# Kernel optimization log

Measured on AMD Instinct MI355X. Metric: run time of the kernel, lower is better.

Reference implementation:

```python
import jax, jax.numpy as jnp
import numpy as np

D_MODEL = 1024
N_HEADS = 16
D_K = D_MODEL // N_HEADS
B, L = 8, 512


def setup_inputs() -> dict:
    key = jax.random.key(0)
    ks = jax.random.split(key, 12)
    s = 0.02
    return {
        "q": jax.random.normal(ks[0], (B, L, D_MODEL), jnp.float32),
        "k": jax.random.normal(ks[1], (B, L, D_MODEL), jnp.float32),
        "v": jax.random.normal(ks[2], (B, L, D_MODEL), jnp.float32),
        "rel_pos_emb": jax.random.normal(ks[3], (L, L, D_MODEL), jnp.float32) * s,
        "mask": jnp.ones((1, 1, L, L), jnp.int32),
        "Wq": jax.random.normal(ks[4], (D_MODEL, D_MODEL), jnp.float32) * s,
        "bq": jnp.zeros((D_MODEL,), jnp.float32),
        "Wk": jax.random.normal(ks[5], (D_MODEL, D_MODEL), jnp.float32) * s,
        "bk": jnp.zeros((D_MODEL,), jnp.float32),
        "Wv": jax.random.normal(ks[6], (D_MODEL, D_MODEL), jnp.float32) * s,
        "bv": jnp.zeros((D_MODEL,), jnp.float32),
        "Wo": jax.random.normal(ks[7], (D_MODEL, D_MODEL), jnp.float32) * s,
        "bo": jnp.zeros((D_MODEL,), jnp.float32),
    }


def reference(q, k, v, rel_pos_emb, mask, Wq, bq, Wk, bk, Wv, bv, Wo, bo):
    Bn, Ln, D = q.shape
    H, dk = N_HEADS, D // N_HEADS
    # QKV projections (nn.Linear: x @ W^T + b), split heads -> [B,H,L,dk]
    qh = (q @ Wq.T + bq).reshape(Bn, Ln, H, dk).transpose(0, 2, 1, 3)
    kh = (k @ Wk.T + bk).reshape(Bn, Ln, H, dk).transpose(0, 2, 1, 3)
    vh = (v @ Wv.T + bv).reshape(Bn, Ln, H, dk).transpose(0, 2, 1, 3)
    # relative position embeddings -> [H,L,L,dk]
    rel = rel_pos_emb.reshape(Ln, Ln, H, dk).transpose(2, 0, 1, 3)
    scale = 1.0 / jnp.sqrt(jnp.float32(dk))
    scores = jnp.einsum('bhld,bhrd->bhlr', qh, kh) * scale
    scores = scores + jnp.einsum('bhld,hlrd->bhlr', qh, rel)
    scores = jnp.where(mask == 0, jnp.float32(-1e9), scores)
    attn = jax.nn.softmax(scores, axis=-1)  # dropout omitted (eval mode)
    out = jnp.einsum('bhlr,bhrd->bhld', attn, vh)
    out = out.transpose(0, 2, 1, 3).reshape(Bn, Ln, D)
    return out @ Wo.T + bo
```

## Files before the change

### kernel.cpp

```cpp
#include <hip/hip_runtime.h>

typedef __attribute__((ext_vector_type(8))) short short8;
typedef __attribute__((ext_vector_type(4))) float f32x4;
typedef __attribute__((ext_vector_type(4))) unsigned short u16x4;
typedef unsigned int u32;
typedef unsigned short ushort_t;

union frag_u { u32 w[4]; short8 s; };

static __device__ __forceinline__ unsigned short f2bf(float x) {
  union { float f; unsigned u; } v; v.f = x;
  unsigned r = v.u + 0x7fffu + ((v.u >> 16) & 1u);
  return (unsigned short)(r >> 16);
}
static __device__ __forceinline__ float bf2f(unsigned short h) {
  union { unsigned u; float f; } v; v.u = ((unsigned)h) << 16;
  return v.f;
}
static __device__ __forceinline__ u32 pk_bf16(float a, float b) {
  u32 r;
  asm("v_cvt_pk_bf16_f32 %0, %1, %2" : "=v"(r) : "v"(a), "v"(b));
  return r;
}

static __device__ __forceinline__ void gl_lds16(const void* g, void* s) {
  __builtin_amdgcn_global_load_lds(
      (const __attribute__((address_space(1))) void*)g,
      (__attribute__((address_space(3))) void*)s, 16, 0, 0);
}

__global__ __launch_bounds__(256) void to_bf16(const float* __restrict__ src,
                                               ushort_t* __restrict__ dst, int n4) {
  int i = blockIdx.x * blockDim.x + threadIdx.x;
  int stride = gridDim.x * blockDim.x;
  for (; i < n4; i += stride) {
    float4 x = *(const float4*)&src[i * 4];
    u16x4 o;
    o.x = f2bf(x.x); o.y = f2bf(x.y); o.z = f2bf(x.z); o.w = f2bf(x.w);
    *(u16x4*)&dst[i * 4] = o;
  }
}

__global__ __launch_bounds__(256) void split3_bf16(const float* __restrict__ src,
                                                   ushort_t* __restrict__ dst, int n) {
  int i = blockIdx.x * blockDim.x + threadIdx.x;
  int stride = gridDim.x * blockDim.x;
  for (; i < n; i += stride) {
    int r = i >> 10, c = i & 1023;
    float x = src[i];
    unsigned short hi = f2bf(x);
    unsigned short lo = f2bf(x - bf2f(hi));
    ushort_t* row = dst + (size_t)r * 3072;
    row[c] = hi; row[1024 + c] = hi; row[2048 + c] = lo;
  }
}

__global__ __launch_bounds__(256) void gemm_qkv(
    const ushort_t* __restrict__ qbf, const ushort_t* __restrict__ kbf,
    const ushort_t* __restrict__ vbf, const ushort_t* __restrict__ Wqb,
    const ushort_t* __restrict__ Wkb, const ushort_t* __restrict__ Wvb,
    const float* __restrict__ bq, const float* __restrict__ bk,
    const float* __restrict__ bv, float* __restrict__ qh,
    ushort_t* __restrict__ khb, ushort_t* __restrict__ vT) {
  __shared__ ushort_t As[2][128 * 32];
  __shared__ ushort_t Bs[2][128 * 32];
  const int t = threadIdx.x;
  const int lane = t & 63;
  const int w = t >> 6;
  const int wr = w >> 1, wc = w & 1;
  const int bid = blockIdx.x;
  const int mt = bid / 24, ntg = bid % 24;
  const int which = ntg >> 3, nt = ntg & 7;
  const ushort_t* A  = which == 0 ? qbf : which == 1 ? kbf : vbf;
  const ushort_t* Bw = which == 0 ? Wqb : which == 1 ? Wkb : Wvb;
  const float* bias  = which == 0 ? bq  : which == 1 ? bk  : bv;
  const int m0 = mt * 128, n0 = nt * 128;
  const int r16 = lane & 15, kb = lane >> 4;

  f32x4 acc[4][4];
#pragma unroll
  for (int mi = 0; mi < 4; ++mi)
#pragma unroll
    for (int ni = 0; ni < 4; ++ni) acc[mi][ni] = (f32x4){0.f, 0.f, 0.f, 0.f};

  auto STAGE = [&](int buf, int k0) {
#pragma unroll
    for (int i = 0; i < 2; ++i) {
      int c = i * 256 + t;
      int row = c >> 2, kc = (c & 3) * 8;
      gl_lds16(&A[(size_t)(m0 + row) * 1024 + k0 + kc], &As[buf][c * 8]);
      gl_lds16(&Bw[(size_t)(n0 + row) * 1024 + k0 + kc], &Bs[buf][c * 8]);
    }
  };

  STAGE(0, 0);
  __syncthreads();
  int cur = 0;
  for (int kt = 0; kt < 32; ++kt) {
    if (kt + 1 < 32) STAGE(cur ^ 1, (kt + 1) * 32);
    short8 af[4], bf[4];
#pragma unroll
    for (int mi = 0; mi < 4; ++mi)
      af[mi] = *(const short8*)&As[cur][(wr * 64 + mi * 16 + r16) * 32 + kb * 8];
#pragma unroll
    for (int ni = 0; ni < 4; ++ni)
      bf[ni] = *(const short8*)&Bs[cur][(wc * 64 + ni * 16 + r16) * 32 + kb * 8];
#pragma unroll
    for (int mi = 0; mi < 4; ++mi)
#pragma unroll
      for (int ni = 0; ni < 4; ++ni)
        acc[mi][ni] = __builtin_amdgcn_mfma_f32_16x16x32_bf16(af[mi], bf[ni], acc[mi][ni], 0, 0, 0);
    __syncthreads();
    cur ^= 1;
  }

  const int rowD = (lane >> 4) * 4;
#pragma unroll
  for (int mi = 0; mi < 4; ++mi) {
#pragma unroll
    for (int ni = 0; ni < 4; ++ni) {
      int n = n0 + wc * 64 + ni * 16 + (lane & 15);
      float bv4 = bias[n];
      int mbase = m0 + wr * 64 + mi * 16 + rowD;
      float vals[4];
#pragma unroll
      for (int j = 0; j < 4; ++j) vals[j] = acc[mi][ni][j] + bv4;
      int hh = n >> 6, d = n & 63;
      if (which == 0) {
#pragma unroll
        for (int j = 0; j < 4; ++j) {
          int m = mbase + j;
          int b = m >> 9, l = m & 511;
          qh[(((size_t)(b * 16 + hh)) * 512 + l) * 64 + d] = vals[j];
        }
      } else if (which == 1) {
#pragma unroll
        for (int j = 0; j < 4; ++j) {
          int m = mbase + j;
          int b = m >> 9, r = m & 511;
          khb[(((size_t)(b * 16 + hh)) * 512 + r) * 64 + d] = f2bf(vals[j]);
        }
      } else {
        int b = mbase >> 9, r = mbase & 511;
        u16x4 pkv;
        pkv.x = f2bf(vals[0]); pkv.y = f2bf(vals[1]);
        pkv.z = f2bf(vals[2]); pkv.w = f2bf(vals[3]);
        *(u16x4*)&vT[(((size_t)(b * 16 + hh)) * 64 + d) * 512 + r] = pkv;
      }
    }
  }
}

__global__ __launch_bounds__(256) void gemm_out(const ushort_t* __restrict__ A,
                                                const ushort_t* __restrict__ Bw,
                                                const float* __restrict__ bias,
                                                float* __restrict__ Cout) {
  __shared__ ushort_t As[2][128 * 32];
  __shared__ ushort_t Bs[2][128 * 32];
  const int t = threadIdx.x;
  const int lane = t & 63;
  const int w = t >> 6;
  const int wr = w >> 1, wc = w & 1;
  const int mt = blockIdx.x >> 3, nt = blockIdx.x & 7;
  const int m0 = mt * 128, n0 = nt * 128;
  const int r16 = lane & 15, kb = lane >> 4;

  f32x4 acc[4][4];
#pragma unroll
  for (int mi = 0; mi < 4; ++mi)
#pragma unroll
    for (int ni = 0; ni < 4; ++ni) acc[mi][ni] = (f32x4){0.f, 0.f, 0.f, 0.f};

  auto STAGE = [&](int buf, int k0) {
#pragma unroll
    for (int i = 0; i < 2; ++i) {
      int c = i * 256 + t;
      int row = c >> 2, kc = (c & 3) * 8;
      gl_lds16(&A[(size_t)(m0 + row) * 3072 + k0 + kc], &As[buf][c * 8]);
      gl_lds16(&Bw[(size_t)(n0 + row) * 3072 + k0 + kc], &Bs[buf][c * 8]);
    }
  };

  STAGE(0, 0);
  __syncthreads();
  int cur = 0;
  for (int kt = 0; kt < 96; ++kt) {
    if (kt + 1 < 96) STAGE(cur ^ 1, (kt + 1) * 32);
    short8 af[4], bf[4];
#pragma unroll
    for (int mi = 0; mi < 4; ++mi)
      af[mi] = *(const short8*)&As[cur][(wr * 64 + mi * 16 + r16) * 32 + kb * 8];
#pragma unroll
    for (int ni = 0; ni < 4; ++ni)
      bf[ni] = *(const short8*)&Bs[cur][(wc * 64 + ni * 16 + r16) * 32 + kb * 8];
#pragma unroll
    for (int mi = 0; mi < 4; ++mi)
#pragma unroll
      for (int ni = 0; ni < 4; ++ni)
        acc[mi][ni] = __builtin_amdgcn_mfma_f32_16x16x32_bf16(af[mi], bf[ni], acc[mi][ni], 0, 0, 0);
    __syncthreads();
    cur ^= 1;
  }

  const int rowD = (lane >> 4) * 4;
#pragma unroll
  for (int mi = 0; mi < 4; ++mi) {
#pragma unroll
    for (int ni = 0; ni < 4; ++ni) {
      int n = n0 + wc * 64 + ni * 16 + (lane & 15);
      float bv = bias[n];
      int mbase = m0 + wr * 64 + mi * 16 + rowD;
#pragma unroll
      for (int j = 0; j < 4; ++j)
        Cout[(size_t)(mbase + j) * 1024 + n] = acc[mi][ni][j] + bv;
    }
  }
}

__global__ __launch_bounds__(256, 2) void attn_mfma(
    const float* __restrict__ qh, const ushort_t* __restrict__ khb,
    const ushort_t* __restrict__ vT, const float* __restrict__ rel,
    const int* __restrict__ mask, ushort_t* __restrict__ Abig) {
  __shared__ ushort_t qs[8][16][64];
  __shared__ float sp2[2][8][17][20];
  const int t = threadIdx.x;
  const int w = t >> 6, lane = t & 63, lh = lane & 15, lg = lane >> 4;
  const int bid = blockIdx.x;
  const int slot = bid & 7, grp = bid >> 3;
  const int h = slot * 2 + (grp & 1);
  const int l0 = (grp >> 1) * 16;
  const int b0 = w * 2;

  {
    int idx = t * 32;
    int b = idx >> 10, l = (idx >> 6) & 15, d0 = idx & 63;
    const float* src = &qh[(((size_t)(b * 16 + h)) * 512 + l0 + l) * 64 + d0];
    int xr = (l & 7) ^ b;
#pragma unroll
    for (int jj = 0; jj < 4; ++jj) {
      f32x4 x0 = *(const f32x4*)&src[jj * 8];
      f32x4 x1 = *(const f32x4*)&src[jj * 8 + 4];
      frag_u fu;
      fu.w[0] = pk_bf16(x0[0], x0[1]); fu.w[1] = pk_bf16(x0[2], x0[3]);
      fu.w[2] = pk_bf16(x1[0], x1[1]); fu.w[3] = pk_bf16(x1[2], x1[3]);
      int pos = ((d0 >> 3) + jj) ^ xr;
      *(short8*)&qs[b][l][pos * 8] = fu.s;
    }
  }

  f32x4 R[16];
  auto LOAD_REL = [&](int r0_) {
#pragma unroll
    for (int li = 0; li < 4; ++li) {
      const float* rp = &rel[((size_t)(l0 + w * 4 + li) * 512 + r0_ + lh) * 1024 + h * 64 + lg * 8];
#pragma unroll
      for (int kb = 0; kb < 2; ++kb) {
        R[li * 4 + kb * 2 + 0] = *(const f32x4*)&rp[kb * 32];
        R[li * 4 + kb * 2 + 1] = *(const f32x4*)&rp[kb * 32 + 4];
      }
    }
  };
  LOAD_REL(0);

  f32x4 O[2][4];
#pragma unroll
  for (int i = 0; i < 2; ++i)
#pragma unroll
    for (int j = 0; j < 4; ++j) O[i][j] = (f32x4){0.f, 0.f, 0.f, 0.f};
  float m_run[2] = {-1e30f, -1e30f}, s_run[2] = {0.f, 0.f};

  __syncthreads();

  for (int it = 0; it < 32; ++it) {
    const int r0 = it * 16;
    const int cur = it & 1;

    short8 kf[2][2], vf[2][4];
#pragma unroll
    for (int bh = 0; bh < 2; ++bh) {
#pragma unroll
      for (int kb = 0; kb < 2; ++kb)
        kf[bh][kb] = *(const short8*)&khb[(((size_t)((b0 + bh) * 16 + h)) * 512 + r0 + lh) * 64 + kb * 32 + lg * 8];
#pragma unroll
      for (int dt = 0; dt < 4; ++dt)
        vf[bh][dt] = *(const short8*)&vT[(((size_t)((b0 + bh) * 16 + h)) * 64 + dt * 16 + lh) * 512 + r0 + lg * 8];
    }
    int4 mk = *(const int4*)&mask[(size_t)(l0 + lh) * 512 + r0 + lg * 4];

#pragma unroll
    for (int li = 0; li < 4; ++li) {
      frag_u a0, a1;
      f32x4 v00 = R[li * 4 + 0], v01 = R[li * 4 + 1];
      f32x4 v10 = R[li * 4 + 2], v11 = R[li * 4 + 3];
      a0.w[0] = pk_bf16(v00[0], v00[1]); a0.w[1] = pk_bf16(v00[2], v00[3]);
      a0.w[2] = pk_bf16(v01[0], v01[1]); a0.w[3] = pk_bf16(v01[2], v01[3]);
      a1.w[0] = pk_bf16(v10[0], v10[1]); a1.w[1] = pk_bf16(v10[2], v10[3]);
      a1.w[2] = pk_bf16(v11[0], v11[1]); a1.w[3] = pk_bf16(v11[2], v11[3]);
      int l = w * 4 + li;
      int xr2 = (l & 7) ^ (lh & 7);
      short8 q0 = *(const short8*)&qs[lh & 7][l][(lg ^ xr2) * 8];
      short8 q1 = *(const short8*)&qs[lh & 7][l][((4 + lg) ^ xr2) * 8];
      f32x4 acc = (f32x4){0.f, 0.f, 0.f, 0.f};
      acc = __builtin_amdgcn_mfma_f32_16x16x32_bf16(a0.s, q0, acc, 0, 0, 0);
      acc = __builtin_amdgcn_mfma_f32_16x16x32_bf16(a1.s, q1, acc, 0, 0, 0);
      if (lh < 8) *(f32x4*)&sp2[cur][lh][l][lg * 4] = acc;
    }
    if (it < 31) LOAD_REL(r0 + 16);
    __syncthreads();

    __builtin_amdgcn_s_setprio(1);
#pragma unroll
    for (int bh = 0; bh < 2; ++bh) {
      int xqk = (lh & 7) ^ (b0 + bh);
      short8 qb0 = *(const short8*)&qs[b0 + bh][lh][(lg ^ xqk) * 8];
      short8 qb1 = *(const short8*)&qs[b0 + bh][lh][((4 + lg) ^ xqk) * 8];
      f32x4 s1 = (f32x4){0.f, 0.f, 0.f, 0.f};
      s1 = __builtin_amdgcn_mfma_f32_16x16x32_bf16(kf[bh][0], qb0, s1, 0, 0, 0);
      s1 = __builtin_amdgcn_mfma_f32_16x16x32_bf16(kf[bh][1], qb1, s1, 0, 0, 0);
      f32x4 s2 = *(const f32x4*)&sp2[cur][b0 + bh][lh][lg * 4];
      f32x4 S;
      S[0] = (mk.x == 0) ? -1e9f : (s1[0] * 0.125f + s2[0]);
      S[1] = (mk.y == 0) ? -1e9f : (s1[1] * 0.125f + s2[1]);
      S[2] = (mk.z == 0) ? -1e9f : (s1[2] * 0.125f + s2[2]);
      S[3] = (mk.w == 0) ? -1e9f : (s1[3] * 0.125f + s2[3]);
      float mt = fmaxf(fmaxf(S[0], S[1]), fmaxf(S[2], S[3]));
      mt = fmaxf(mt, __shfl_xor(mt, 16));
      mt = fmaxf(mt, __shfl_xor(mt, 32));
      float mn = fmaxf(m_run[bh], mt);
      float fsc = __expf(m_run[bh] - mn);
      f32x4 P;
      P[0] = __expf(S[0] - mn); P[1] = __expf(S[1] - mn);
      P[2] = __expf(S[2] - mn); P[3] = __expf(S[3] - mn);
      float ps = P[0] + P[1] + P[2] + P[3];
      ps += __shfl_xor(ps, 16);
      ps += __shfl_xor(ps, 32);
      s_run[bh] = s_run[bh] * fsc + ps;
      m_run[bh] = mn;
#pragma unroll
      for (int dt = 0; dt < 4; ++dt) O[bh][dt] *= fsc;
      u32 pk0 = pk_bf16(P[0], P[1]), pk1 = pk_bf16(P[2], P[3]);
      int s0l = (lh + 32 * lg) & 63;
      u32 w0 = (u32)__shfl((int)pk0, s0l), w1 = (u32)__shfl((int)pk1, s0l);
      u32 w2 = (u32)__shfl((int)pk0, s0l + 16), w3 = (u32)__shfl((int)pk1, s0l + 16);
      bool vld = (lg < 2);
      frag_u pb;
      pb.w[0] = vld ? w0 : 0u; pb.w[1] = vld ? w1 : 0u;
      pb.w[2] = vld ? w2 : 0u; pb.w[3] = vld ? w3 : 0u;
#pragma unroll
      for (int dt = 0; dt < 4; ++dt)
        O[bh][dt] = __builtin_amdgcn_mfma_f32_16x16x32_bf16(vf[bh][dt], pb.s, O[bh][dt], 0, 0, 0);
    }
    __builtin_amdgcn_s_setprio(0);
  }

#pragma unroll
  for (int bh = 0; bh < 2; ++bh) {
    float inv = 1.0f / s_run[bh];
    ushort_t* rowp = &Abig[(size_t)((b0 + bh) * 512 + l0 + lh) * 3072];
#pragma unroll
    for (int dt = 0; dt < 4; ++dt) {
      int c = h * 64 + dt * 16 + lg * 4;
      f32x4 o = O[bh][dt];
      float x0 = o[0] * inv, x1 = o[1] * inv, x2 = o[2] * inv, x3 = o[3] * inv;
      u16x4 hi, lo;
      hi.x = f2bf(x0); lo.x = f2bf(x0 - bf2f(hi.x));
      hi.y = f2bf(x1); lo.y = f2bf(x1 - bf2f(hi.y));
      hi.z = f2bf(x2); lo.z = f2bf(x2 - bf2f(hi.z));
      hi.w = f2bf(x3); lo.w = f2bf(x3 - bf2f(hi.w));
      *(u16x4*)&rowp[c] = hi;
      *(u16x4*)&rowp[1024 + c] = lo;
      *(u16x4*)&rowp[2048 + c] = hi;
    }
  }
}

extern "C" void kernel_launch(void* const* d_in, const int* in_sizes, int n_in,
                              void* d_out, int out_size, void* d_ws, size_t ws_size,
                              hipStream_t stream) {
  const float* q    = (const float*)d_in[0];
  const float* k    = (const float*)d_in[1];
  const float* v    = (const float*)d_in[2];
  const float* rel  = (const float*)d_in[3];
  const int*   mask = (const int*)d_in[4];
  const float* Wq   = (const float*)d_in[5];
  const float* bq   = (const float*)d_in[6];
  const float* Wk   = (const float*)d_in[7];
  const float* bk   = (const float*)d_in[8];
  const float* Wv   = (const float*)d_in[9];
  const float* bv   = (const float*)d_in[10];
  const float* Wo   = (const float*)d_in[11];
  const float* bo   = (const float*)d_in[12];
  float* out = (float*)d_out;

  char* ws = (char*)d_ws;
  float*    qh  = (float*)(ws);
  ushort_t* khb = (ushort_t*)(ws + 16777216);
  ushort_t* vT  = (ushort_t*)(ws + 16777216 + 8388608);
  ushort_t* X   = (ushort_t*)(ws + 33554432);
  ushort_t* Y   = (ushort_t*)(ws + 58720256);
  ushort_t* qbf = X;
  ushort_t* kbf = X + 4194304;
  ushort_t* vbf = X + 8388608;
  ushort_t* Wqb = Y;
  ushort_t* Wkb = Y + 1048576;
  ushort_t* Wvb = Y + 2097152;

  to_bf16<<<1024, 256, 0, stream>>>(q, qbf, 1048576);
  to_bf16<<<1024, 256, 0, stream>>>(k, kbf, 1048576);
  to_bf16<<<1024, 256, 0, stream>>>(v, vbf, 1048576);
  to_bf16<<<256, 256, 0, stream>>>(Wq, Wqb, 262144);
  to_bf16<<<256, 256, 0, stream>>>(Wk, Wkb, 262144);
  to_bf16<<<256, 256, 0, stream>>>(Wv, Wvb, 262144);

  gemm_qkv<<<768, 256, 0, stream>>>(qbf, kbf, vbf, Wqb, Wkb, Wvb,
                                    bq, bk, bv, qh, khb, vT);

  split3_bf16<<<1024, 256, 0, stream>>>(Wo, Y, 1048576);

  attn_mfma<<<512, 256, 0, stream>>>(qh, khb, vT, rel, mask, X);

  gemm_out<<<256, 256, 0, stream>>>(X, Y, bo, out);
}
```

Before: 438.8 us.

## Double-buffer rel prefetch two tiles ahead, stagger key order, merge bf16 converts

The attention kernel now keeps two register buffers of relative-position data and prefetches two key tiles ahead. Each prefetch is issued after the barrier, behind a sched_barrier, so it overlaps the QK/softmax/PV work. Each block starts its key loop at a different rotated offset so blocks spread their reads of the large rel tensor across memory channels. The six separate fp32-to-bf16 conversion launches are merged into two multi-source launches. In exchange the doubled rel buffers raise register pressure, which could spill or hurt occupancy at the launch-bound of 2 blocks per CU.

```diff
diff --git a/kernel.cpp b/kernel.cpp
--- a/kernel.cpp
+++ b/kernel.cpp
@@ -29,15 +29,21 @@
       (__attribute__((address_space(3))) void*)s, 16, 0, 0);
 }
 
-__global__ __launch_bounds__(256) void to_bf16(const float* __restrict__ src,
-                                               ushort_t* __restrict__ dst, int n4) {
+__global__ __launch_bounds__(256) void to_bf16_3(const float* __restrict__ s0,
+                                                 const float* __restrict__ s1,
+                                                 const float* __restrict__ s2,
+                                                 ushort_t* __restrict__ dst,
+                                                 int lg2, int n4) {
   int i = blockIdx.x * blockDim.x + threadIdx.x;
   int stride = gridDim.x * blockDim.x;
   for (; i < n4; i += stride) {
-    float4 x = *(const float4*)&src[i * 4];
+    int which = i >> lg2;
+    const float* s = which == 0 ? s0 : which == 1 ? s1 : s2;
+    int local = i - (which << lg2);
+    float4 x = *(const float4*)&s[(size_t)local * 4];
     u16x4 o;
     o.x = f2bf(x.x); o.y = f2bf(x.y); o.z = f2bf(x.z); o.w = f2bf(x.w);
-    *(u16x4*)&dst[i * 4] = o;
+    *(u16x4*)&dst[(size_t)i * 4] = o;
   }
 }
 
@@ -230,6 +236,7 @@
   const int h = slot * 2 + (grp & 1);
   const int l0 = (grp >> 1) * 16;
   const int b0 = w * 2;
+  const int off = (grp * 5) & 31;
 
   {
     int idx = t * 32;
@@ -248,11 +255,12 @@
     }
   }
 
-  f32x4 R[16];
-  auto LOAD_REL = [&](int r0_) {
+  f32x4 RA[16], RB[16];
+  const float* relbase = &rel[(size_t)(l0 + w * 4) * 512 * 1024 + h * 64 + lg * 8];
+  auto LOAD_REL = [&](f32x4 (&R)[16], int r0_) {
 #pragma unroll
     for (int li = 0; li < 4; ++li) {
-      const float* rp = &rel[((size_t)(l0 + w * 4 + li) * 512 + r0_ + lh) * 1024 + h * 64 + lg * 8];
+      const float* rp = relbase + ((size_t)li * 512 + r0_ + lh) * 1024;
 #pragma unroll
       for (int kb = 0; kb < 2; ++kb) {
         R[li * 4 + kb * 2 + 0] = *(const f32x4*)&rp[kb * 32];
@@ -260,7 +268,8 @@
       }
     }
   };
-  LOAD_REL(0);
+  LOAD_REL(RA, off * 16);
+  LOAD_REL(RB, ((off + 1) & 31) * 16);
 
   f32x4 O[2][4];
 #pragma unroll
@@ -271,8 +280,8 @@
 
   __syncthreads();
 
-  for (int it = 0; it < 32; ++it) {
-    const int r0 = it * 16;
+  auto BODY = [&](f32x4 (&R)[16], int it) {
+    const int r0 = ((it + off) & 31) * 16;
     const int cur = it & 1;
 
     short8 kf[2][2], vf[2][4];
@@ -305,8 +314,9 @@
       acc = __builtin_amdgcn_mfma_f32_16x16x32_bf16(a1.s, q1, acc, 0, 0, 0);
       if (lh < 8) *(f32x4*)&sp2[cur][lh][l][lg * 4] = acc;
     }
-    if (it < 31) LOAD_REL(r0 + 16);
     __syncthreads();
+    __builtin_amdgcn_sched_barrier(0);
+    if (it < 30) LOAD_REL(R, ((it + 2 + off) & 31) * 16);
 
     __builtin_amdgcn_s_setprio(1);
 #pragma unroll
@@ -351,6 +361,12 @@
         O[bh][dt] = __builtin_amdgcn_mfma_f32_16x16x32_bf16(vf[bh][dt], pb.s, O[bh][dt], 0, 0, 0);
     }
     __builtin_amdgcn_s_setprio(0);
+  };
+
+#pragma unroll 1
+  for (int it2 = 0; it2 < 32; it2 += 2) {
+    BODY(RA, it2);
+    BODY(RB, it2 + 1);
   }
 
 #pragma unroll
@@ -405,12 +421,8 @@
   ushort_t* Wkb = Y + 1048576;
   ushort_t* Wvb = Y + 2097152;
 
-  to_bf16<<<1024, 256, 0, stream>>>(q, qbf, 1048576);
-  to_bf16<<<1024, 256, 0, stream>>>(k, kbf, 1048576);
-  to_bf16<<<1024, 256, 0, stream>>>(v, vbf, 1048576);
-  to_bf16<<<256, 256, 0, stream>>>(Wq, Wqb, 262144);
-  to_bf16<<<256, 256, 0, stream>>>(Wk, Wkb, 262144);
-  to_bf16<<<256, 256, 0, stream>>>(Wv, Wvb, 262144);
+  to_bf16_3<<<1536, 256, 0, stream>>>(q, k, v, X, 20, 3145728);
+  to_bf16_3<<<384, 256, 0, stream>>>(Wq, Wk, Wv, Y, 18, 786432);
 
   gemm_qkv<<<768, 256, 0, stream>>>(qbf, kbf, vbf, Wqb, Wkb, Wvb,
                                     bq, bk, bv, qh, khb, vT);
```

After: 548.5 us. 1.25x slower.
